# Kernel tuning notes

Hardware: AMD Instinct MI355X
Metric: run time of the kernel (lower is better)

Reference implementation:

```python
import jax, jax.numpy as jnp
import numpy as np

B, C, N, H = 4, 256, 4096, 4
DK = C // H


def _proj(x, w, b):
    # Conv1d with kernel size 1 == per-point linear: [B,C,N] x [O,C] -> [B,O,N]
    return jnp.einsum('oc,bcn->bon', w, x) + b[None, :, None]


def setup_inputs() -> dict:
    key = jax.random.key(0)
    ks = jax.random.split(key, 9)
    s = 1.0 / np.sqrt(C)
    return {
        'x': jax.random.normal(ks[0], (B, C, N), jnp.float32),
        'wq': jax.random.normal(ks[1], (C, C), jnp.float32) * s,
        'bq': jax.random.normal(ks[2], (C,), jnp.float32) * 0.01,
        'wk': jax.random.normal(ks[3], (C, C), jnp.float32) * s,
        'bk': jax.random.normal(ks[4], (C,), jnp.float32) * 0.01,
        'wv': jax.random.normal(ks[5], (C, C), jnp.float32) * s,
        'bv': jax.random.normal(ks[6], (C,), jnp.float32) * 0.01,
        'wp': jax.random.normal(ks[7], (C, C), jnp.float32) * s,
        'bp': jax.random.normal(ks[8], (C,), jnp.float32) * 0.01,
    }


def reference(x, wq, bq, wk, bk, wv, bv, wp, bp):
    b, c, n = x.shape
    q = _proj(x, wq, bq).reshape(b, H, DK, n)
    k = _proj(x, wk, bk).reshape(b, H, DK, n)
    v = _proj(x, wv, bv).reshape(b, H, DK, n)
    scale = 1.0 / jnp.sqrt(jnp.asarray(DK, x.dtype))
    # scores over point pairs: [B,H,N,N]
    scores = jnp.einsum('bhdn,bhdm->bhnm', q, k) * scale
    attn = jax.nn.softmax(scores, axis=-1)
    out = jnp.einsum('bhnm,bhdm->bhdn', attn, v)  # [B,H,DK,N]
    out = out.reshape(b, c, n)
    out = _proj(out, wp, bp)
    return out + x
```

## Files before the change

kernel.cpp:

```cpp
#include <hip/hip_runtime.h>


#define BDIM 4
#define CDIM 256
#define NDIM 4096
#define HDIM 4
#define DKDIM 64
#define NQ   (BDIM * HDIM * NDIM)
#define NSPLIT 2
#define KPERZ (NDIM / NSPLIT)
#define QSCALE 0.18033688011112042f
#define WSZ (CDIM * CDIM)

typedef __bf16 bf16x8 __attribute__((ext_vector_type(8)));
typedef float f32x4 __attribute__((ext_vector_type(4)));
typedef short s16x4 __attribute__((ext_vector_type(4)));
typedef unsigned short u16;
typedef unsigned int u32;

__device__ __forceinline__ u16 f2bf(float f) {
  union { __bf16 h; u16 s; } u; u.h = (__bf16)f; return u.s;
}
__device__ __forceinline__ float bf2f(u16 v) {
  union { u32 u; float f; } x; x.u = (u32)v << 16; return x.f;
}
__device__ __forceinline__ u32 pk2(float a, float b) {
  return (u32)f2bf(a) | ((u32)f2bf(b) << 16);
}
__device__ __forceinline__ void gload16(const u16* g, u16* l) {
  __builtin_amdgcn_global_load_lds(
      (const __attribute__((address_space(1))) void*)g,
      (__attribute__((address_space(3))) void*)l, 16, 0, 0);
}

__global__ __launch_bounds__(256) void wconv_kernel(
    const float* __restrict__ wq, const float* __restrict__ wk,
    const float* __restrict__ wv, const float* __restrict__ wp,
    u16* __restrict__ wb)
{
  const int a = blockIdx.y;
  const float* src = (a == 0) ? wq : (a == 1) ? wk : (a == 2) ? wv : wp;
  const float sc = (a == 0) ? QSCALE : 1.0f;
  const int i = (blockIdx.x * 256 + threadIdx.x) * 8;
  const float4 v0 = *(const float4*)(src + i);
  const float4 v1 = *(const float4*)(src + i + 4);
  union { u32 p[4]; uint4 q; } o;
  o.p[0] = pk2(v0.x * sc, v0.y * sc);
  o.p[1] = pk2(v0.z * sc, v0.w * sc);
  o.p[2] = pk2(v1.x * sc, v1.y * sc);
  o.p[3] = pk2(v1.z * sc, v1.w * sc);
  *(uint4*)(wb + (size_t)a * WSZ + i) = o.q;
}

__global__ __launch_bounds__(256) void xt_kernel(
    const float* __restrict__ x, u16* __restrict__ xT)
{
  const int b = blockIdx.z, c0 = blockIdx.y * 64, n0 = blockIdx.x * 64;
  __shared__ __align__(16) float T[64][68];
  const int t = threadIdx.x;
  {
    const int cr = t >> 4, nc = (t & 15) * 4;
    #pragma unroll
    for (int ci = 0; ci < 4; ++ci) {
      const float4 v = *(const float4*)&x[((size_t)(b * CDIM + c0 + cr + ci * 16)) * NDIM + n0 + nc];
      *(float4*)&T[cr + ci * 16][nc] = v;
    }
  }
  __syncthreads();
  {
    const int n = t >> 2, g = t & 3;
    union { u16 u[16]; uint4 v[2]; } pk;
    #pragma unroll
    for (int u_ = 0; u_ < 16; ++u_) pk.u[u_] = f2bf(T[g * 16 + u_][n]);
    uint4* dst = (uint4*)&xT[((size_t)(b * NDIM + n0 + n)) * CDIM + c0 + g * 16];
    dst[0] = pk.v[0]; dst[1] = pk.v[1];
  }
}

__global__ __launch_bounds__(256, 3) void qkv_kernel(
    const u16* __restrict__ xT, const u16* __restrict__ wb,
    const float* __restrict__ bq, const float* __restrict__ bk,
    const float* __restrict__ bv,
    u16* __restrict__ qT, u16* __restrict__ kT, u16* __restrict__ vB)
{
  const int b = blockIdx.z;
  const int p = blockIdx.y;
  const int n0 = blockIdx.x * 64;
  const float* bsel = (p == 0) ? bq : (p == 1) ? bk : bv;
  const float wscale = (p == 0) ? QSCALE : 1.0f;

  __shared__ __align__(16) u16 XTs[64][264];
  const int t = threadIdx.x, lane = t & 63, w = t >> 6;
  const int qd = lane >> 4, lm = lane & 15;
  const int sr = t >> 2, sg = (t & 3) * 8;

  {
    const u16* xsrc = xT + ((size_t)(b * NDIM + n0 + sr)) * CDIM + sg;
    #pragma unroll
    for (int cs = 0; cs < 8; ++cs)
      *(uint4*)&XTs[sr][cs * 32 + sg] = *(const uint4*)(xsrc + cs * 32);
  }
  __syncthreads();

  const u16* wrow = wb + (size_t)p * WSZ + (size_t)(64 * w + lm) * CDIM + qd * 8;

  f32x4 acc[4][4];
  #pragma unroll
  for (int nt = 0; nt < 4; ++nt)
    #pragma unroll
    for (int j = 0; j < 4; ++j) acc[nt][j] = (f32x4){0.f, 0.f, 0.f, 0.f};

  #pragma unroll
  for (int cs = 0; cs < 8; ++cs) {
    bf16x8 wf[4];
    #pragma unroll
    for (int j = 0; j < 4; ++j)
      wf[j] = *(const bf16x8*)(wrow + (size_t)(16 * j) * CDIM + cs * 32);
    bf16x8 xf[4];
    #pragma unroll
    for (int nt = 0; nt < 4; ++nt)
      xf[nt] = *(const bf16x8*)&XTs[16 * nt + lm][cs * 32 + qd * 8];
    #pragma unroll
    for (int nt = 0; nt < 4; ++nt)
      #pragma unroll
      for (int j = 0; j < 4; ++j) {
        if (p < 2)
          acc[nt][j] = __builtin_amdgcn_mfma_f32_16x16x32_bf16(xf[nt], wf[j], acc[nt][j], 0, 0, 0);
        else
          acc[nt][j] = __builtin_amdgcn_mfma_f32_16x16x32_bf16(wf[j], xf[nt], acc[nt][j], 0, 0, 0);
      }
  }

  if (p < 2) {
    u16* out = (p == 0) ? qT : kT;
    #pragma unroll
    for (int j = 0; j < 4; ++j) {
      const int og = 64 * w + 16 * j + lm;
      const float bv2 = bsel[og] * wscale;
      #pragma unroll
      for (int nt = 0; nt < 4; ++nt)
        #pragma unroll
        for (int r = 0; r < 4; ++r) {
          const int n = n0 + 16 * nt + 4 * qd + r;
          out[((size_t)(b * NDIM + n)) * CDIM + og] = f2bf(acc[nt][j][r] + bv2);
        }
    }
  } else {
    #pragma unroll
    for (int j = 0; j < 4; ++j) {
      const float4 b4 = *(const float4*)&bsel[64 * w + 16 * j + 4 * qd];
      const float bvr[4] = {b4.x, b4.y, b4.z, b4.w};
      #pragma unroll
      for (int nt = 0; nt < 4; ++nt)
        #pragma unroll
        for (int r = 0; r < 4; ++r) {
          const int og = 64 * w + 16 * j + 4 * qd + r;
          const int n = n0 + 16 * nt + lm;
          vB[((size_t)(b * CDIM + og)) * NDIM + n] = f2bf(acc[nt][j][r] + bvr[r]);
        }
    }
  }
}

__global__ __launch_bounds__(256, 4) void attn_kernel(
    const u16* __restrict__ qT, const u16* __restrict__ kT,
    const u16* __restrict__ vB, u16* __restrict__ Opart,
    float* __restrict__ Lp)
{
  const int bh = blockIdx.y, b = bh >> 2, h = bh & 3;
  const int n0 = blockIdx.x * 128;
  const int z  = blockIdx.z;

  __shared__ __align__(16) u16 KVlds[2][2][64][64];

  const int t = threadIdx.x, lane = t & 63, w = t >> 6;
  const int qd = lane >> 4, lm = lane & 15, l7 = lm & 7;

  bf16x8 qf[2][2];
  {
    const u16* qbase = qT + ((size_t)(b * NDIM) + n0) * CDIM + h * 64;
    #pragma unroll
    for (int s = 0; s < 2; ++s)
      #pragma unroll
      for (int hh = 0; hh < 2; ++hh)
        qf[s][hh] = *(const bf16x8*)(qbase +
            (size_t)(16 * (2 * w + s) + lm) * CDIM + 32 * hh + qd * 8);
  }

  const s16x4 ones = (s16x4){(short)0x3F80, (short)0x3F80, (short)0x3F80, (short)0x3F80};
  f32x4 la[2];
  la[0] = (f32x4){0.f, 0.f, 0.f, 0.f};
  la[1] = (f32x4){0.f, 0.f, 0.f, 0.f};

  f32x4 oa[2][4];
  #pragma unroll
  for (int s = 0; s < 2; ++s)
    #pragma unroll
    for (int dt = 0; dt < 4; ++dt) oa[s][dt] = (f32x4){0.f, 0.f, 0.f, 0.f};

  const int srow = lane >> 3;
  const int swz  = 8 * ((lane & 7) ^ srow);
  const u16* kp0 = kT + ((size_t)(b * NDIM + z * KPERZ + 8 * w + srow)) * CDIM + h * 64 + swz;
  const u16* kp1 = kp0 + (size_t)32 * CDIM;
  const u16* vp0 = vB + ((size_t)(b * CDIM + h * 64 + 8 * w + srow)) * NDIM + z * KPERZ + swz;
  const u16* vp1 = vp0 + (size_t)32 * NDIM;

  {
    u16* kb = &KVlds[0][0][0][0];
    u16* vb2 = &KVlds[0][1][0][0];
    gload16(kp0, kb + w * 512);
    gload16(kp1, kb + (4 + w) * 512);
    gload16(vp0, vb2 + w * 512);
    gload16(vp1, vb2 + (4 + w) * 512);
  }

  #pragma unroll 1
  for (int it = 0; it < KPERZ / 64; ++it) {
    __syncthreads();
    if (it + 1 < KPERZ / 64) {
      const size_t ko = (size_t)(it + 1) * 64 * CDIM;
      const int    vo = (it + 1) * 64;
      u16* kb = &KVlds[(it + 1) & 1][0][0][0];
      u16* vb2 = &KVlds[(it + 1) & 1][1][0][0];
      gload16(kp0 + ko, kb + w * 512);
      gload16(kp1 + ko, kb + (4 + w) * 512);
      gload16(vp0 + vo, vb2 + w * 512);
      gload16(vp1 + vo, vb2 + (4 + w) * 512);
    }
    const u16 (*Kt)[64] = KVlds[it & 1][0];
    const u16 (*Vt)[64] = KVlds[it & 1][1];

    union { u16 u[4]; u32 d[2]; s16x4 v; } pk[2][4];

    #pragma unroll
    for (int nt = 0; nt < 4; ++nt) {
      const bf16x8 kf0 = *(const bf16x8*)&Kt[16 * nt + lm][8 * (qd ^ l7)];
      const bf16x8 kf1 = *(const bf16x8*)&Kt[16 * nt + lm][8 * ((4 + qd) ^ l7)];
      #pragma unroll
      for (int s = 0; s < 2; ++s) {
        f32x4 zz = (f32x4){0.f, 0.f, 0.f, 0.f};
        zz = __builtin_amdgcn_mfma_f32_16x16x32_bf16(kf0, qf[s][0], zz, 0, 0, 0);
        zz = __builtin_amdgcn_mfma_f32_16x16x32_bf16(kf1, qf[s][1], zz, 0, 0, 0);
        const float p0 = __builtin_amdgcn_exp2f(zz[0]);
        const float p1 = __builtin_amdgcn_exp2f(zz[1]);
        const float p2 = __builtin_amdgcn_exp2f(zz[2]);
        const float p3 = __builtin_amdgcn_exp2f(zz[3]);
        pk[s][nt].d[0] = pk2(p0, p1);
        pk[s][nt].d[1] = pk2(p2, p3);
      }
    }

    #pragma unroll
    for (int c = 0; c < 4; ++c) {
      s16x4 av[4];
      #pragma unroll
      for (int dt = 0; dt < 4; ++dt)
        av[dt] = *(const s16x4*)&Vt[16 * dt + lm][(16 * c + 4 * qd) ^ (8 * l7)];
      la[0] = __builtin_amdgcn_mfma_f32_16x16x16bf16_1k(ones, pk[0][c].v, la[0], 0, 0, 0);
      la[1] = __builtin_amdgcn_mfma_f32_16x16x16bf16_1k(ones, pk[1][c].v, la[1], 0, 0, 0);
      #pragma unroll
      for (int dt = 0; dt < 4; ++dt) {
        oa[0][dt] = __builtin_amdgcn_mfma_f32_16x16x16bf16_1k(av[dt], pk[0][c].v, oa[0][dt], 0, 0, 0);
        oa[1][dt] = __builtin_amdgcn_mfma_f32_16x16x16bf16_1k(av[dt], pk[1][c].v, oa[1][dt], 0, 0, 0);
      }
    }
  }

  const float l_i[2] = {la[0][0], la[1][0]};

  __syncthreads();
  u16 (*Ot)[72] = (u16(*)[72])&KVlds[0][0][0][0];
  #pragma unroll
  for (int s = 0; s < 2; ++s) {
    const float inv = 1.0f / l_i[s];
    #pragma unroll
    for (int dt = 0; dt < 4; ++dt)
      #pragma unroll
      for (int r = 0; r < 4; ++r)
        Ot[16 * (2 * w + s) + lm][16 * dt + 4 * qd + r] = f2bf(oa[s][dt][r] * inv);
  }
  if (qd == 0) {
    const size_t lbase = ((size_t)z * (BDIM * HDIM) + bh) * NDIM;
    #pragma unroll
    for (int s = 0; s < 2; ++s)
      Lp[lbase + n0 + 16 * (2 * w + s) + lm] = l_i[s];
  }
  __syncthreads();
  {
    const int r = t >> 1, g = (t & 1) * 32;
    u16* dst = Opart + (((size_t)z * (BDIM * HDIM) + bh) * NDIM + n0 + r) * DKDIM + g;
    const uint4* srcp = (const uint4*)&Ot[r][g];
    uint4* d4 = (uint4*)dst;
    d4[0] = srcp[0]; d4[1] = srcp[1]; d4[2] = srcp[2]; d4[3] = srcp[3];
  }
}

__global__ __launch_bounds__(256, 4) void projout_kernel(
    const u16* __restrict__ Opart, const float* __restrict__ Lp,
    const u16* __restrict__ wb, const float* __restrict__ bp,
    const float* __restrict__ res, float* __restrict__ out)
{
  const int b = blockIdx.z, o0 = blockIdx.y * 128, n0 = blockIdx.x * 64;
  __shared__ __align__(16) u16 XTs[64][40];
  const int t = threadIdx.x, lane = t & 63, w = t >> 6;
  const int qd = lane >> 4, lm = lane & 15;
  const int sr = t >> 2, sg = (t & 3) * 8;

  float wh[4][NSPLIT];
  #pragma unroll
  for (int hh = 0; hh < 4; ++hh) {
    const size_t i0 = ((size_t)(b * HDIM + hh)) * NDIM + n0 + sr;
    float l[NSPLIT], tot = 0.f;
    #pragma unroll
    for (int zz = 0; zz < NSPLIT; ++zz) { l[zz] = Lp[(size_t)zz * NQ + i0]; tot += l[zz]; }
    const float iv = 1.0f / tot;
    #pragma unroll
    for (int zz = 0; zz < NSPLIT; ++zz) wh[hh][zz] = l[zz] * iv;
  }

  const u16* wrow0 = wb + (size_t)3 * WSZ + (size_t)(o0 + 32 * w + lm) * CDIM + qd * 8;
  const u16* wrow1 = wrow0 + (size_t)16 * CDIM;

  f32x4 acc[4][2];
  #pragma unroll
  for (int nt = 0; nt < 4; ++nt)
    #pragma unroll
    for (int j = 0; j < 2; ++j) acc[nt][j] = (f32x4){0.f, 0.f, 0.f, 0.f};

  for (int cs = 0; cs < 8; ++cs) {
    const int c0 = cs * 32;
    const int hh = c0 >> 6;
    const int dk = (c0 & 63) + sg;
    const bf16x8 wf0 = *(const bf16x8*)(wrow0 + c0);
    const bf16x8 wf1 = *(const bf16x8*)(wrow1 + c0);
    __syncthreads();
    {
      const size_t obase = (((size_t)(b * HDIM + hh)) * NDIM + n0 + sr) * DKDIM + dk;
      float v[8] = {0.f, 0.f, 0.f, 0.f, 0.f, 0.f, 0.f, 0.f};
      #pragma unroll
      for (int zz = 0; zz < NSPLIT; ++zz) {
        union { u16 u[8]; uint4 q; } a;
        a.q = *(const uint4*)(Opart + (size_t)zz * NQ * DKDIM + obase);
        const float wz = wh[hh][zz];
        #pragma unroll
        for (int j = 0; j < 8; ++j) v[j] = fmaf(wz, bf2f(a.u[j]), v[j]);
      }
      union { u16 u[8]; uint4 q; } ov;
      #pragma unroll
      for (int j = 0; j < 8; ++j) ov.u[j] = f2bf(v[j]);
      *(uint4*)&XTs[sr][sg] = ov.q;
    }
    __syncthreads();
    bf16x8 xf[4];
    #pragma unroll
    for (int nt = 0; nt < 4; ++nt) xf[nt] = *(const bf16x8*)&XTs[16 * nt + lm][qd * 8];
    #pragma unroll
    for (int nt = 0; nt < 4; ++nt) {
      acc[nt][0] = __builtin_amdgcn_mfma_f32_16x16x32_bf16(wf0, xf[nt], acc[nt][0], 0, 0, 0);
      acc[nt][1] = __builtin_amdgcn_mfma_f32_16x16x32_bf16(wf1, xf[nt], acc[nt][1], 0, 0, 0);
    }
  }

  #pragma unroll
  for (int j = 0; j < 2; ++j) {
    const float4 b4 = *(const float4*)&bp[o0 + 32 * w + 16 * j + 4 * qd];
    const float bvr[4] = {b4.x, b4.y, b4.z, b4.w};
    #pragma unroll
    for (int nt = 0; nt < 4; ++nt)
      #pragma unroll
      for (int r = 0; r < 4; ++r) {
        const int og = o0 + 32 * w + 16 * j + 4 * qd + r;
        const int n = n0 + 16 * nt + lm;
        const size_t idx = ((size_t)(b * CDIM + og)) * NDIM + n;
        out[idx] = acc[nt][j][r] + bvr[r] + res[idx];
      }
  }
}

extern "C" void kernel_launch(void* const* d_in, const int* in_sizes, int n_in,
                              void* d_out, int out_size, void* d_ws, size_t ws_size,
                              hipStream_t stream)
{
  const float* x  = (const float*)d_in[0];
  const float* wq = (const float*)d_in[1];
  const float* bq = (const float*)d_in[2];
  const float* wk = (const float*)d_in[3];
  const float* bk = (const float*)d_in[4];
  const float* wv = (const float*)d_in[5];
  const float* bv = (const float*)d_in[6];
  const float* wp = (const float*)d_in[7];
  const float* bp = (const float*)d_in[8];
  float* out = (float*)d_out;

  const size_t sz = (size_t)BDIM * CDIM * NDIM;
  u16* xTb = (u16*)d_ws;
  u16* qTb = xTb + sz;
  u16* kTb = qTb + sz;
  u16* vBb = kTb + sz;
  u16* Opart = vBb + sz;
  float* Lp = (float*)(Opart + (size_t)NSPLIT * sz);
  u16* wbf = (u16*)(Lp + (size_t)NSPLIT * NQ);

  const dim3 blk(256);
  wconv_kernel<<<dim3(WSZ / (256 * 8), 4, 1), blk, 0, stream>>>(wq, wk, wv, wp, wbf);
  xt_kernel<<<dim3(NDIM / 64, CDIM / 64, BDIM), blk, 0, stream>>>(x, xTb);
  qkv_kernel<<<dim3(NDIM / 64, 3, BDIM), blk, 0, stream>>>(
      xTb, wbf, bq, bk, bv, qTb, kTb, vBb);
  attn_kernel<<<dim3(NDIM / 128, BDIM * HDIM, NSPLIT), blk, 0, stream>>>(
      qTb, kTb, vBb, Opart, Lp);
  projout_kernel<<<dim3(NDIM / 64, 2, BDIM), blk, 0, stream>>>(
      Opart, Lp, wbf, bp, x, out);
}
```

Measured before the change: 201.8 us.

## Fuse x transpose and weight bf16 conversion into projection kernels

```diff
diff --git a/kernel.cpp b/kernel.cpp
--- a/kernel.cpp
+++ b/kernel.cpp
@@ -10,7 +10,6 @@
 #define NSPLIT 2
 #define KPERZ (NDIM / NSPLIT)
 #define QSCALE 0.18033688011112042f
-#define WSZ (CDIM * CDIM)
 
 typedef __bf16 bf16x8 __attribute__((ext_vector_type(8)));
 typedef float f32x4 __attribute__((ext_vector_type(4)));
@@ -33,76 +32,48 @@
       (__attribute__((address_space(3))) void*)l, 16, 0, 0);
 }
 
-__global__ __launch_bounds__(256) void wconv_kernel(
-    const float* __restrict__ wq, const float* __restrict__ wk,
-    const float* __restrict__ wv, const float* __restrict__ wp,
-    u16* __restrict__ wb)
-{
-  const int a = blockIdx.y;
-  const float* src = (a == 0) ? wq : (a == 1) ? wk : (a == 2) ? wv : wp;
-  const float sc = (a == 0) ? QSCALE : 1.0f;
-  const int i = (blockIdx.x * 256 + threadIdx.x) * 8;
-  const float4 v0 = *(const float4*)(src + i);
-  const float4 v1 = *(const float4*)(src + i + 4);
-  union { u32 p[4]; uint4 q; } o;
-  o.p[0] = pk2(v0.x * sc, v0.y * sc);
-  o.p[1] = pk2(v0.z * sc, v0.w * sc);
-  o.p[2] = pk2(v1.x * sc, v1.y * sc);
-  o.p[3] = pk2(v1.z * sc, v1.w * sc);
-  *(uint4*)(wb + (size_t)a * WSZ + i) = o.q;
-}
-
-__global__ __launch_bounds__(256) void xt_kernel(
-    const float* __restrict__ x, u16* __restrict__ xT)
-{
-  const int b = blockIdx.z, c0 = blockIdx.y * 64, n0 = blockIdx.x * 64;
-  __shared__ __align__(16) float T[64][68];
-  const int t = threadIdx.x;
-  {
-    const int cr = t >> 4, nc = (t & 15) * 4;
-    #pragma unroll
-    for (int ci = 0; ci < 4; ++ci) {
-      const float4 v = *(const float4*)&x[((size_t)(b * CDIM + c0 + cr + ci * 16)) * NDIM + n0 + nc];
-      *(float4*)&T[cr + ci * 16][nc] = v;
-    }
-  }
-  __syncthreads();
-  {
-    const int n = t >> 2, g = t & 3;
-    union { u16 u[16]; uint4 v[2]; } pk;
-    #pragma unroll
-    for (int u_ = 0; u_ < 16; ++u_) pk.u[u_] = f2bf(T[g * 16 + u_][n]);
-    uint4* dst = (uint4*)&xT[((size_t)(b * NDIM + n0 + n)) * CDIM + c0 + g * 16];
-    dst[0] = pk.v[0]; dst[1] = pk.v[1];
-  }
-}
-
 __global__ __launch_bounds__(256, 3) void qkv_kernel(
-    const u16* __restrict__ xT, const u16* __restrict__ wb,
-    const float* __restrict__ bq, const float* __restrict__ bk,
-    const float* __restrict__ bv,
+    const float* __restrict__ x,
+    const float* __restrict__ wq, const float* __restrict__ bq,
+    const float* __restrict__ wk, const float* __restrict__ bk,
+    const float* __restrict__ wv, const float* __restrict__ bv,
     u16* __restrict__ qT, u16* __restrict__ kT, u16* __restrict__ vB)
 {
   const int b = blockIdx.z;
   const int p = blockIdx.y;
   const int n0 = blockIdx.x * 64;
+  const float* wsel = (p == 0) ? wq : (p == 1) ? wk : wv;
   const float* bsel = (p == 0) ? bq : (p == 1) ? bk : bv;
   const float wscale = (p == 0) ? QSCALE : 1.0f;
 
+  __shared__ __align__(16) float T[64][68];
   __shared__ __align__(16) u16 XTs[64][264];
   const int t = threadIdx.x, lane = t & 63, w = t >> 6;
   const int qd = lane >> 4, lm = lane & 15;
-  const int sr = t >> 2, sg = (t & 3) * 8;
-
-  {
-    const u16* xsrc = xT + ((size_t)(b * NDIM + n0 + sr)) * CDIM + sg;
-    #pragma unroll
-    for (int cs = 0; cs < 8; ++cs)
-      *(uint4*)&XTs[sr][cs * 32 + sg] = *(const uint4*)(xsrc + cs * 32);
-  }
-  __syncthreads();
-
-  const u16* wrow = wb + (size_t)p * WSZ + (size_t)(64 * w + lm) * CDIM + qd * 8;
+
+  for (int cc = 0; cc < 4; ++cc) {
+    const int cbase = cc * 64;
+    {
+      const int cr = t >> 4, nc = (t & 15) * 4;
+      #pragma unroll
+      for (int ci = 0; ci < 4; ++ci) {
+        const float4 v = *(const float4*)&x[((size_t)(b * CDIM + cbase + cr + ci * 16)) * NDIM + n0 + nc];
+        *(float4*)&T[cr + ci * 16][nc] = v;
+      }
+    }
+    __syncthreads();
+    {
+      const int n = t >> 2, g = t & 3;
+      union { u16 u[16]; uint4 v[2]; } pk;
+      #pragma unroll
+      for (int u_ = 0; u_ < 16; ++u_) pk.u[u_] = f2bf(T[g * 16 + u_][n]);
+      *(uint4*)&XTs[n][cbase + g * 16]     = pk.v[0];
+      *(uint4*)&XTs[n][cbase + g * 16 + 8] = pk.v[1];
+    }
+    __syncthreads();
+  }
+
+  const float* wrow = wsel + (size_t)(64 * w + lm) * CDIM + qd * 8;
 
   f32x4 acc[4][4];
   #pragma unroll
@@ -114,8 +85,16 @@
   for (int cs = 0; cs < 8; ++cs) {
     bf16x8 wf[4];
     #pragma unroll
-    for (int j = 0; j < 4; ++j)
-      wf[j] = *(const bf16x8*)(wrow + (size_t)(16 * j) * CDIM + cs * 32);
+    for (int j = 0; j < 4; ++j) {
+      const float4 a0 = *(const float4*)(wrow + (size_t)(16 * j) * CDIM + cs * 32);
+      const float4 a1 = *(const float4*)(wrow + (size_t)(16 * j) * CDIM + cs * 32 + 4);
+      union { u32 d[4]; bf16x8 v; } u;
+      u.d[0] = pk2(a0.x * wscale, a0.y * wscale);
+      u.d[1] = pk2(a0.z * wscale, a0.w * wscale);
+      u.d[2] = pk2(a1.x * wscale, a1.y * wscale);
+      u.d[3] = pk2(a1.z * wscale, a1.w * wscale);
+      wf[j] = u.v;
+    }
     bf16x8 xf[4];
     #pragma unroll
     for (int nt = 0; nt < 4; ++nt)
@@ -297,7 +276,7 @@
 
 __global__ __launch_bounds__(256, 4) void projout_kernel(
     const u16* __restrict__ Opart, const float* __restrict__ Lp,
-    const u16* __restrict__ wb, const float* __restrict__ bp,
+    const float* __restrict__ wp, const float* __restrict__ bp,
     const float* __restrict__ res, float* __restrict__ out)
 {
   const int b = blockIdx.z, o0 = blockIdx.y * 128, n0 = blockIdx.x * 64;
@@ -318,8 +297,8 @@
     for (int zz = 0; zz < NSPLIT; ++zz) wh[hh][zz] = l[zz] * iv;
   }
 
-  const u16* wrow0 = wb + (size_t)3 * WSZ + (size_t)(o0 + 32 * w + lm) * CDIM + qd * 8;
-  const u16* wrow1 = wrow0 + (size_t)16 * CDIM;
+  const float* wrow0 = wp + (size_t)(o0 + 32 * w + lm) * CDIM + qd * 8;
+  const float* wrow1 = wrow0 + (size_t)16 * CDIM;
 
   f32x4 acc[4][2];
   #pragma unroll
@@ -331,8 +310,19 @@
     const int c0 = cs * 32;
     const int hh = c0 >> 6;
     const int dk = (c0 & 63) + sg;
-    const bf16x8 wf0 = *(const bf16x8*)(wrow0 + c0);
-    const bf16x8 wf1 = *(const bf16x8*)(wrow1 + c0);
+    bf16x8 wf0, wf1;
+    {
+      const float4 a0 = *(const float4*)(wrow0 + c0);
+      const float4 a1 = *(const float4*)(wrow0 + c0 + 4);
+      const float4 c0v = *(const float4*)(wrow1 + c0);
+      const float4 c1v = *(const float4*)(wrow1 + c0 + 4);
+      union { u32 d[4]; bf16x8 v; } u0, u1;
+      u0.d[0] = pk2(a0.x, a0.y);  u0.d[1] = pk2(a0.z, a0.w);
+      u0.d[2] = pk2(a1.x, a1.y);  u0.d[3] = pk2(a1.z, a1.w);
+      u1.d[0] = pk2(c0v.x, c0v.y); u1.d[1] = pk2(c0v.z, c0v.w);
+      u1.d[2] = pk2(c1v.x, c1v.y); u1.d[3] = pk2(c1v.z, c1v.w);
+      wf0 = u0.v; wf1 = u1.v;
+    }
     __syncthreads();
     {
       const size_t obase = (((size_t)(b * HDIM + hh)) * NDIM + n0 + sr) * DKDIM + dk;
@@ -393,21 +383,17 @@
   float* out = (float*)d_out;
 
   const size_t sz = (size_t)BDIM * CDIM * NDIM;
-  u16* xTb = (u16*)d_ws;
-  u16* qTb = xTb + sz;
+  u16* qTb = (u16*)d_ws;
   u16* kTb = qTb + sz;
   u16* vBb = kTb + sz;
   u16* Opart = vBb + sz;
   float* Lp = (float*)(Opart + (size_t)NSPLIT * sz);
-  u16* wbf = (u16*)(Lp + (size_t)NSPLIT * NQ);
 
   const dim3 blk(256);
-  wconv_kernel<<<dim3(WSZ / (256 * 8), 4, 1), blk, 0, stream>>>(wq, wk, wv, wp, wbf);
-  xt_kernel<<<dim3(NDIM / 64, CDIM / 64, BDIM), blk, 0, stream>>>(x, xTb);
   qkv_kernel<<<dim3(NDIM / 64, 3, BDIM), blk, 0, stream>>>(
-      xTb, wbf, bq, bk, bv, qTb, kTb, vBb);
+      x, wq, bq, wk, bk, wv, bv, qTb, kTb, vBb);
   attn_kernel<<<dim3(NDIM / 128, BDIM * HDIM, NSPLIT), blk, 0, stream>>>(
       qTb, kTb, vBb, Opart, Lp);
   projout_kernel<<<dim3(NDIM / 64, 2, BDIM), blk, 0, stream>>>(
-      Opart, Lp, wbf, bp, x, out);
-}
+      Opart, Lp, wp, bp, x, out);
+}
```

Result: slower. 206.0 us (+2.1%).
